# Optimization experiments

Hardware: AMD Instinct MI355X
Metric: run time of the kernel (lower is better)

The kernel has to match this reference:

```python
import jax, jax.numpy as jnp
import numpy as np

N, INSIZE, K, D = 512, 512, 64, 16


def setup_inputs() -> dict:
    key = jax.random.key(0)
    k1, k2, k3 = jax.random.split(key, 3)
    x = jax.random.normal(k1, (N, INSIZE), dtype=jnp.float32)
    W = jax.random.normal(k2, (K * D, INSIZE), dtype=jnp.float32) * (1.0 / np.sqrt(INSIZE))
    b = jax.random.normal(k3, (K * D,), dtype=jnp.float32) * 0.01
    return {"x": x, "W": W, "b": b}


def reference(x, W, b):
    # Linear: [N, insize] -> [N, K*D] -> [N, K, D]
    feat = (x @ W.T + b).reshape(-1, K, D)
    n = feat.shape[0]
    # Pairwise L1 distance over D: norm[i, k, j] = sum_d |feat[i,k,d] - feat[j,k,d]|
    # feature [N,K,D,1] vs feature_ [1,K,D,N] in the original broadcast
    diff = jnp.abs(feat[:, :, :, None] - jnp.transpose(feat, (1, 2, 0))[None])  # [N,K,D,N]
    norm = jnp.sum(diff, axis=2)  # [N,K,N]
    # Eraser: suppress self-similarity on the diagonal with a large penalty
    eraser = jnp.eye(n, dtype=feat.dtype)[:, None, :]  # [N,1,N]
    c_b = jnp.exp(-(norm + eraser * 1e6))
    o_b = jnp.sum(c_b, axis=2)  # [N,K]
    return jnp.concatenate((x, o_b), axis=1)  # [N, insize+K]
```

## Files before the change

kernel.cpp:

```cpp
#include <hip/hip_runtime.h>

#define NPTS 512
#define INS  512
#define KDIM 64
#define DDIM 16
#define CDIM (KDIM*DDIM)
#define OUTC (INS + KDIM)
#define KSPLIT 8
#define FEAT_ELEMS ((size_t)NPTS * CDIM)
#define FEAT_F4    (FEAT_ELEMS / 4)

__device__ __forceinline__ float exp2_fast(float x) {
    return __builtin_amdgcn_exp2f(x);
}

__device__ __forceinline__ void fma2(float2& acc, float s, float x, float y) {
    acc.x = __builtin_fmaf(s, x, acc.x);
    acc.y = __builtin_fmaf(s, y, acc.y);
}

__global__ __launch_bounds__(256) void gemm_kernel(
    const float* __restrict__ x,
    const float* __restrict__ W,
    float* __restrict__ featT)
{
    const int tid = threadIdx.x;
    const int cbase = blockIdx.x * 64;
    const int ibase = blockIdx.y * 64;
    const int kbase = blockIdx.z * (INS / KSPLIT);

    __shared__ float xs[16][68];
    __shared__ float wss[16][68];

    const int tx = tid & 15;
    const int ty = tid >> 4;
    const int kkL = tid & 15;
    const int rL  = tid >> 4;

    float2 acc[4][2] = {};

    for (int k0 = kbase; k0 < kbase + INS / KSPLIT; k0 += 16) {
        #pragma unroll
        for (int q = 0; q < 4; ++q) {
            xs[kkL][rL + 16 * q]  = x[(ibase + rL + 16 * q) * INS + k0 + kkL];
            wss[kkL][rL + 16 * q] = W[(cbase + rL + 16 * q) * INS + k0 + kkL];
        }
        __syncthreads();

        #pragma unroll
        for (int kk = 0; kk < 16; ++kk) {
            float4 a = *(const float4*)&xs[kk][ty * 4];
            float4 w = *(const float4*)&wss[kk][tx * 4];
            fma2(acc[0][0], a.x, w.x, w.y);  fma2(acc[0][1], a.x, w.z, w.w);
            fma2(acc[1][0], a.y, w.x, w.y);  fma2(acc[1][1], a.y, w.z, w.w);
            fma2(acc[2][0], a.z, w.x, w.y);  fma2(acc[2][1], a.z, w.z, w.w);
            fma2(acc[3][0], a.w, w.x, w.y);  fma2(acc[3][1], a.w, w.z, w.w);
        }
        __syncthreads();
    }

    const int c = cbase + tx * 4;
    const int k = c >> 4;
    const int d = c & 15;
    float* dst = featT + (size_t)blockIdx.z * FEAT_ELEMS;
    #pragma unroll
    for (int ii = 0; ii < 4; ++ii) {
        const int i = ibase + ty * 4 + ii;
        float4 v = make_float4(acc[ii][0].x, acc[ii][0].y, acc[ii][1].x, acc[ii][1].y);
        *(float4*)&dst[((size_t)k * NPTS + i) * DDIM + d] = v;
    }
}

__global__ __launch_bounds__(256) void fuse_reduce_init_kernel(
    const float* __restrict__ featT,
    const float* __restrict__ bias,
    const float* __restrict__ x,
    float* __restrict__ featR,
    float* __restrict__ out)
{
    const int b = blockIdx.x;
    if (b < 512) {
        const int f4 = b * 256 + threadIdx.x;
        const float4* s = (const float4*)featT;
        float4 p0 = s[f4];
        float4 p1 = s[f4 + 1 * FEAT_F4];
        float4 p2 = s[f4 + 2 * FEAT_F4];
        float4 p3 = s[f4 + 3 * FEAT_F4];
        float4 p4 = s[f4 + 4 * FEAT_F4];
        float4 p5 = s[f4 + 5 * FEAT_F4];
        float4 p6 = s[f4 + 6 * FEAT_F4];
        float4 p7 = s[f4 + 7 * FEAT_F4];
        const int k = f4 >> 11;
        const float4 bq = ((const float4*)bias)[(k << 2) + (f4 & 3)];
        const float LOG2E = 1.4426950408889634f;
        float4 r;
        r.x = (((p0.x + p1.x) + (p2.x + p3.x)) + ((p4.x + p5.x) + (p6.x + p7.x)) + bq.x) * LOG2E;
        r.y = (((p0.y + p1.y) + (p2.y + p3.y)) + ((p4.y + p5.y) + (p6.y + p7.y)) + bq.y) * LOG2E;
        r.z = (((p0.z + p1.z) + (p2.z + p3.z)) + ((p4.z + p5.z) + (p6.z + p7.z)) + bq.z) * LOG2E;
        r.w = (((p0.w + p1.w) + (p2.w + p3.w)) + ((p4.w + p5.w) + (p6.w + p7.w)) + bq.w) * LOG2E;
        ((float4*)featR)[f4] = r;
    } else {
        const int idx = (b - 512) * 256 + threadIdx.x;
        const int i  = idx / (OUTC / 4);
        const int j4 = idx - i * (OUTC / 4);
        float4 v;
        if (j4 < INS / 4) v = ((const float4*)x)[i * (INS / 4) + j4];
        else              v = make_float4(-1.0f, -1.0f, -1.0f, -1.0f);
        ((float4*)out)[idx] = v;
    }
}

__global__ __launch_bounds__(256, 4) void pairwise_kernel(
    const float* __restrict__ featR,
    float* __restrict__ out)
{
    const int k     = blockIdx.x;
    const int itile = blockIdx.y;
    const int jq    = blockIdx.z;

    __shared__ float fj[64 * DDIM];
    __shared__ float part[4][256];

    ((float4*)fj)[threadIdx.x] =
        ((const float4*)(featR + ((size_t)k * NPTS + jq * 64) * DDIM))[threadIdx.x];

    const int lane = threadIdx.x & 63;
    const int wv   = threadIdx.x >> 6;

    float fi[4][16];
    #pragma unroll
    for (int u = 0; u < 4; ++u) {
        const int i = itile * 256 + u * 64 + lane;
        const float4* p = (const float4*)(featR + ((size_t)k * NPTS + i) * DDIM);
        float4 v0 = p[0], v1 = p[1], v2 = p[2], v3 = p[3];
        fi[u][0]=v0.x;  fi[u][1]=v0.y;  fi[u][2]=v0.z;  fi[u][3]=v0.w;
        fi[u][4]=v1.x;  fi[u][5]=v1.y;  fi[u][6]=v1.z;  fi[u][7]=v1.w;
        fi[u][8]=v2.x;  fi[u][9]=v2.y;  fi[u][10]=v2.z; fi[u][11]=v2.w;
        fi[u][12]=v3.x; fi[u][13]=v3.y; fi[u][14]=v3.z; fi[u][15]=v3.w;
    }
    __syncthreads();

    float acc[4] = {0.f, 0.f, 0.f, 0.f};
    const float* fp = fj + wv * 16 * DDIM;
    #pragma unroll 2
    for (int jj = 0; jj < 16; ++jj) {
        const float* p = fp + jj * DDIM;
        float4 q0 = *(const float4*)(p);
        float4 q1 = *(const float4*)(p + 4);
        float4 q2 = *(const float4*)(p + 8);
        float4 q3 = *(const float4*)(p + 12);
        #pragma unroll
        for (int u = 0; u < 4; ++u) {
            float a0 = fabsf(fi[u][0]  - q0.x) + fabsf(fi[u][1]  - q0.y)
                     + fabsf(fi[u][2]  - q0.z) + fabsf(fi[u][3]  - q0.w);
            float a1 = fabsf(fi[u][4]  - q1.x) + fabsf(fi[u][5]  - q1.y)
                     + fabsf(fi[u][6]  - q1.z) + fabsf(fi[u][7]  - q1.w);
            float a2 = fabsf(fi[u][8]  - q2.x) + fabsf(fi[u][9]  - q2.y)
                     + fabsf(fi[u][10] - q2.z) + fabsf(fi[u][11] - q2.w);
            float a3 = fabsf(fi[u][12] - q3.x) + fabsf(fi[u][13] - q3.y)
                     + fabsf(fi[u][14] - q3.z) + fabsf(fi[u][15] - q3.w);
            acc[u] += exp2_fast(-((a0 + a1) + (a2 + a3)));
        }
    }

    #pragma unroll
    for (int u = 0; u < 4; ++u)
        part[wv][u * 64 + lane] = acc[u];
    __syncthreads();

    {
        const int t = threadIdx.x;
        float s = (part[0][t] + part[1][t]) + (part[2][t] + part[3][t]);
        const int i = itile * 256 + t;
        atomicAdd(&out[(size_t)i * OUTC + INS + k], s);
    }
}

extern "C" void kernel_launch(void* const* d_in, const int* in_sizes, int n_in,
                              void* d_out, int out_size, void* d_ws, size_t ws_size,
                              hipStream_t stream) {
    const float* x    = (const float*)d_in[0];
    const float* W    = (const float*)d_in[1];
    const float* bias = (const float*)d_in[2];
    float* out = (float*)d_out;
    float* featT = (float*)d_ws;
    float* featR = featT + KSPLIT * FEAT_ELEMS;

    gemm_kernel<<<dim3(CDIM / 64, NPTS / 64, KSPLIT), 256, 0, stream>>>(x, W, featT);
    fuse_reduce_init_kernel<<<dim3(512 + NPTS * (OUTC / 4) / 256), 256, 0, stream>>>(
        featT, bias, x, featR, out);
    pairwise_kernel<<<dim3(KDIM, 2, 8), 256, 0, stream>>>(featR, out);
}
```

Before: 109.0 us.

## Use bf16 MFMA GEMM with prepacking and fold split-K reduction into pairwise

Replaces the FP32 SIMT GEMM with a bf16 MFMA 16x16x32 GEMM that reads x and W prepacked into bf16 by a new kernel. Split-K drops to 4 and bias plus the LOG2E scale are applied in the GEMM epilogue. The pairwise kernel now sums the four split-K partials itself, which removes the separate reduction kernel and its featR buffer. Rounding features to bf16 can cause accuracy problems, because exp(-L1) is sensitive to feature error, and the pairwise kernel now repeats the partial-sum loads for every block that reads the same rows.

```diff
diff --git a/kernel.cpp b/kernel.cpp
--- a/kernel.cpp
+++ b/kernel.cpp
@@ -6,101 +6,48 @@
 #define DDIM 16
 #define CDIM (KDIM*DDIM)
 #define OUTC (INS + KDIM)
-#define KSPLIT 8
+#define KSPLIT 4
 #define FEAT_ELEMS ((size_t)NPTS * CDIM)
-#define FEAT_F4    (FEAT_ELEMS / 4)
+#define LOG2E 1.4426950408889634f
+
+typedef short short8 __attribute__((ext_vector_type(8)));
+typedef float f32x4  __attribute__((ext_vector_type(4)));
 
 __device__ __forceinline__ float exp2_fast(float x) {
     return __builtin_amdgcn_exp2f(x);
 }
 
-__device__ __forceinline__ void fma2(float2& acc, float s, float x, float y) {
-    acc.x = __builtin_fmaf(s, x, acc.x);
-    acc.y = __builtin_fmaf(s, y, acc.y);
-}
-
-__global__ __launch_bounds__(256) void gemm_kernel(
-    const float* __restrict__ x,
-    const float* __restrict__ W,
-    float* __restrict__ featT)
-{
-    const int tid = threadIdx.x;
-    const int cbase = blockIdx.x * 64;
-    const int ibase = blockIdx.y * 64;
-    const int kbase = blockIdx.z * (INS / KSPLIT);
-
-    __shared__ float xs[16][68];
-    __shared__ float wss[16][68];
-
-    const int tx = tid & 15;
-    const int ty = tid >> 4;
-    const int kkL = tid & 15;
-    const int rL  = tid >> 4;
-
-    float2 acc[4][2] = {};
-
-    for (int k0 = kbase; k0 < kbase + INS / KSPLIT; k0 += 16) {
-        #pragma unroll
-        for (int q = 0; q < 4; ++q) {
-            xs[kkL][rL + 16 * q]  = x[(ibase + rL + 16 * q) * INS + k0 + kkL];
-            wss[kkL][rL + 16 * q] = W[(cbase + rL + 16 * q) * INS + k0 + kkL];
-        }
-        __syncthreads();
-
-        #pragma unroll
-        for (int kk = 0; kk < 16; ++kk) {
-            float4 a = *(const float4*)&xs[kk][ty * 4];
-            float4 w = *(const float4*)&wss[kk][tx * 4];
-            fma2(acc[0][0], a.x, w.x, w.y);  fma2(acc[0][1], a.x, w.z, w.w);
-            fma2(acc[1][0], a.y, w.x, w.y);  fma2(acc[1][1], a.y, w.z, w.w);
-            fma2(acc[2][0], a.z, w.x, w.y);  fma2(acc[2][1], a.z, w.z, w.w);
-            fma2(acc[3][0], a.w, w.x, w.y);  fma2(acc[3][1], a.w, w.z, w.w);
-        }
-        __syncthreads();
-    }
-
-    const int c = cbase + tx * 4;
-    const int k = c >> 4;
-    const int d = c & 15;
-    float* dst = featT + (size_t)blockIdx.z * FEAT_ELEMS;
-    #pragma unroll
-    for (int ii = 0; ii < 4; ++ii) {
-        const int i = ibase + ty * 4 + ii;
-        float4 v = make_float4(acc[ii][0].x, acc[ii][0].y, acc[ii][1].x, acc[ii][1].y);
-        *(float4*)&dst[((size_t)k * NPTS + i) * DDIM + d] = v;
-    }
-}
-
-__global__ __launch_bounds__(256) void fuse_reduce_init_kernel(
-    const float* __restrict__ featT,
-    const float* __restrict__ bias,
-    const float* __restrict__ x,
-    float* __restrict__ featR,
-    float* __restrict__ out)
+__device__ __forceinline__ unsigned int f2bf(float f) {
+    unsigned int x = __float_as_uint(f);
+    return (x + 0x7fffu + ((x >> 16) & 1u)) >> 16;
+}
+
+__device__ __forceinline__ uint4 cvt8(const float* src) {
+    float4 lo = *(const float4*)src;
+    float4 hi = *(const float4*)(src + 4);
+    uint4 v;
+    v.x = f2bf(lo.x) | (f2bf(lo.y) << 16);
+    v.y = f2bf(lo.z) | (f2bf(lo.w) << 16);
+    v.z = f2bf(hi.x) | (f2bf(hi.y) << 16);
+    v.w = f2bf(hi.z) | (f2bf(hi.w) << 16);
+    return v;
+}
+
+__global__ __launch_bounds__(256) void prepack_kernel(
+    const float* __restrict__ x, const float* __restrict__ W,
+    uint4* __restrict__ xP, uint4* __restrict__ WP, float* __restrict__ out)
 {
     const int b = blockIdx.x;
-    if (b < 512) {
-        const int f4 = b * 256 + threadIdx.x;
-        const float4* s = (const float4*)featT;
-        float4 p0 = s[f4];
-        float4 p1 = s[f4 + 1 * FEAT_F4];
-        float4 p2 = s[f4 + 2 * FEAT_F4];
-        float4 p3 = s[f4 + 3 * FEAT_F4];
-        float4 p4 = s[f4 + 4 * FEAT_F4];
-        float4 p5 = s[f4 + 5 * FEAT_F4];
-        float4 p6 = s[f4 + 6 * FEAT_F4];
-        float4 p7 = s[f4 + 7 * FEAT_F4];
-        const int k = f4 >> 11;
-        const float4 bq = ((const float4*)bias)[(k << 2) + (f4 & 3)];
-        const float LOG2E = 1.4426950408889634f;
-        float4 r;
-        r.x = (((p0.x + p1.x) + (p2.x + p3.x)) + ((p4.x + p5.x) + (p6.x + p7.x)) + bq.x) * LOG2E;
-        r.y = (((p0.y + p1.y) + (p2.y + p3.y)) + ((p4.y + p5.y) + (p6.y + p7.y)) + bq.y) * LOG2E;
-        r.z = (((p0.z + p1.z) + (p2.z + p3.z)) + ((p4.z + p5.z) + (p6.z + p7.z)) + bq.z) * LOG2E;
-        r.w = (((p0.w + p1.w) + (p2.w + p3.w)) + ((p4.w + p5.w) + (p6.w + p7.w)) + bq.w) * LOG2E;
-        ((float4*)featR)[f4] = r;
+    if (b < 128) {
+        const int t = b * 256 + threadIdx.x;
+        const int kc = t & 63, i = t >> 6;
+        xP[kc * NPTS + i] = cvt8(x + i * INS + kc * 8);
+    } else if (b < 384) {
+        const int t = (b - 128) * 256 + threadIdx.x;
+        const int kc = t & 63, c = t >> 6;
+        WP[kc * CDIM + c] = cvt8(W + c * INS + kc * 8);
     } else {
-        const int idx = (b - 512) * 256 + threadIdx.x;
+        const int idx = (b - 384) * 256 + threadIdx.x;
         const int i  = idx / (OUTC / 4);
         const int j4 = idx - i * (OUTC / 4);
         float4 v;
@@ -110,19 +57,104 @@
     }
 }
 
+__global__ __launch_bounds__(256) void mfma_gemm_kernel(
+    const uint4* __restrict__ xP, const uint4* __restrict__ WP,
+    const float* __restrict__ bias, float* __restrict__ featT)
+{
+    __shared__ uint4 As[16 * 64];
+    __shared__ uint4 Bs[16 * 64];
+
+    const int tid   = threadIdx.x;
+    const int cbase = blockIdx.x * 64;
+    const int ibase = blockIdx.y * 64;
+    const int kc0   = blockIdx.z * 16;
+
+    #pragma unroll
+    for (int r = 0; r < 4; ++r) {
+        const int idx = r * 256 + tid;
+        const int kc = idx >> 6, col = idx & 63;
+        As[idx] = xP[(kc0 + kc) * NPTS + ibase + col];
+        Bs[idx] = WP[(kc0 + kc) * CDIM + cbase + col];
+    }
+    __syncthreads();
+
+    const int lane = tid & 63, wv = tid >> 6;
+    const int quad = lane >> 4, ln = lane & 15;
+
+    f32x4 acc[4];
+    #pragma unroll
+    for (int mi = 0; mi < 4; ++mi) acc[mi] = (f32x4){0.f, 0.f, 0.f, 0.f};
+
+    #pragma unroll
+    for (int t = 0; t < 4; ++t) {
+        uint4 bu = Bs[(t * 4 + quad) * 64 + wv * 16 + ln];
+        short8 bf = *(short8*)&bu;
+        #pragma unroll
+        for (int mi = 0; mi < 4; ++mi) {
+            uint4 au = As[(t * 4 + quad) * 64 + mi * 16 + ln];
+            short8 af = *(short8*)&au;
+            acc[mi] = __builtin_amdgcn_mfma_f32_16x16x32_bf16(af, bf, acc[mi], 0, 0, 0);
+        }
+    }
+
+    const int kg = (cbase >> 4) + wv;
+    float badd = 0.f;
+    if (blockIdx.z == 0) badd = bias[cbase + wv * 16 + ln];
+    float* dst = featT + (size_t)blockIdx.z * FEAT_ELEMS
+               + ((size_t)kg * NPTS) * DDIM + ln;
+    #pragma unroll
+    for (int mi = 0; mi < 4; ++mi) {
+        #pragma unroll
+        for (int reg = 0; reg < 4; ++reg) {
+            const int i = ibase + mi * 16 + quad * 4 + reg;
+            dst[(size_t)i * DDIM] = (acc[mi][reg] + badd) * LOG2E;
+        }
+    }
+}
+
+__device__ __forceinline__ float4 sum4(const float4* s0, const float4* s1,
+                                       const float4* s2, const float4* s3, size_t g) {
+    float4 a = s0[g], b = s1[g], c = s2[g], d = s3[g];
+    float4 r;
+    r.x = (a.x + b.x) + (c.x + d.x);
+    r.y = (a.y + b.y) + (c.y + d.y);
+    r.z = (a.z + b.z) + (c.z + d.z);
+    r.w = (a.w + b.w) + (c.w + d.w);
+    return r;
+}
+
 __global__ __launch_bounds__(256, 4) void pairwise_kernel(
-    const float* __restrict__ featR,
+    const float* __restrict__ f0, const float* __restrict__ f1,
+    const float* __restrict__ f2, const float* __restrict__ f3,
     float* __restrict__ out)
 {
     const int k     = blockIdx.x;
     const int itile = blockIdx.y;
     const int jq    = blockIdx.z;
 
-    __shared__ float fj[64 * DDIM];
-    __shared__ float part[4][256];
-
-    ((float4*)fj)[threadIdx.x] =
-        ((const float4*)(featR + ((size_t)k * NPTS + jq * 64) * DDIM))[threadIdx.x];
+    __shared__ float4 fj4[64 * 4];
+    __shared__ float4 fiL[16 * 64];
+    __shared__ float  part[4][256];
+
+    const float4* s0 = (const float4*)f0;
+    const float4* s1 = (const float4*)f1;
+    const float4* s2 = (const float4*)f2;
+    const float4* s3 = (const float4*)f3;
+
+    {
+        const size_t g = ((size_t)k * NPTS + jq * 64) * 4 + threadIdx.x;
+        fj4[threadIdx.x] = sum4(s0, s1, s2, s3, g);
+    }
+    {
+        const size_t base = ((size_t)k * NPTS + itile * 256) * 4;
+        #pragma unroll
+        for (int r = 0; r < 4; ++r) {
+            const int idx = r * 256 + threadIdx.x;
+            const int il = idx >> 2, q = idx & 3;
+            fiL[((il >> 6) * 4 + q) * 64 + (il & 63)] = sum4(s0, s1, s2, s3, base + idx);
+        }
+    }
+    __syncthreads();
 
     const int lane = threadIdx.x & 63;
     const int wv   = threadIdx.x >> 6;
@@ -130,25 +162,22 @@
     float fi[4][16];
     #pragma unroll
     for (int u = 0; u < 4; ++u) {
-        const int i = itile * 256 + u * 64 + lane;
-        const float4* p = (const float4*)(featR + ((size_t)k * NPTS + i) * DDIM);
-        float4 v0 = p[0], v1 = p[1], v2 = p[2], v3 = p[3];
-        fi[u][0]=v0.x;  fi[u][1]=v0.y;  fi[u][2]=v0.z;  fi[u][3]=v0.w;
-        fi[u][4]=v1.x;  fi[u][5]=v1.y;  fi[u][6]=v1.z;  fi[u][7]=v1.w;
-        fi[u][8]=v2.x;  fi[u][9]=v2.y;  fi[u][10]=v2.z; fi[u][11]=v2.w;
-        fi[u][12]=v3.x; fi[u][13]=v3.y; fi[u][14]=v3.z; fi[u][15]=v3.w;
-    }
-    __syncthreads();
+        #pragma unroll
+        for (int q = 0; q < 4; ++q) {
+            float4 v = fiL[(u * 4 + q) * 64 + lane];
+            fi[u][q * 4 + 0] = v.x; fi[u][q * 4 + 1] = v.y;
+            fi[u][q * 4 + 2] = v.z; fi[u][q * 4 + 3] = v.w;
+        }
+    }
 
     float acc[4] = {0.f, 0.f, 0.f, 0.f};
-    const float* fp = fj + wv * 16 * DDIM;
+    const float4* fp = fj4 + wv * 16 * 4;
     #pragma unroll 2
     for (int jj = 0; jj < 16; ++jj) {
-        const float* p = fp + jj * DDIM;
-        float4 q0 = *(const float4*)(p);
-        float4 q1 = *(const float4*)(p + 4);
-        float4 q2 = *(const float4*)(p + 8);
-        float4 q3 = *(const float4*)(p + 12);
+        float4 q0 = fp[jj * 4 + 0];
+        float4 q1 = fp[jj * 4 + 1];
+        float4 q2 = fp[jj * 4 + 2];
+        float4 q3 = fp[jj * 4 + 3];
         #pragma unroll
         for (int u = 0; u < 4; ++u) {
             float a0 = fabsf(fi[u][0]  - q0.x) + fabsf(fi[u][1]  - q0.y)
@@ -183,11 +212,13 @@
     const float* W    = (const float*)d_in[1];
     const float* bias = (const float*)d_in[2];
     float* out = (float*)d_out;
+
     float* featT = (float*)d_ws;
-    float* featR = featT + KSPLIT * FEAT_ELEMS;
-
-    gemm_kernel<<<dim3(CDIM / 64, NPTS / 64, KSPLIT), 256, 0, stream>>>(x, W, featT);
-    fuse_reduce_init_kernel<<<dim3(512 + NPTS * (OUTC / 4) / 256), 256, 0, stream>>>(
-        featT, bias, x, featR, out);
-    pairwise_kernel<<<dim3(KDIM, 2, 8), 256, 0, stream>>>(featR, out);
-}
+    uint4* xP = (uint4*)(featT + KSPLIT * FEAT_ELEMS);
+    uint4* WP = xP + 64 * NPTS;
+
+    prepack_kernel<<<dim3(672), 256, 0, stream>>>(x, W, xP, WP, out);
+    mfma_gemm_kernel<<<dim3(16, 8, 4), 256, 0, stream>>>(xP, WP, bias, featT);
+    pairwise_kernel<<<dim3(KDIM, 2, 8), 256, 0, stream>>>(
+        featT, featT + FEAT_ELEMS, featT + 2 * FEAT_ELEMS, featT + 3 * FEAT_ELEMS, out);
+}
```

Result: faster. 101.0 us (-7.4%).
